# Optimization experiments

Measured on AMD Instinct MI355X. Metric: run time of the kernel, lower is better.

The kernel has to match this reference:

```python
import jax, jax.numpy as jnp
import numpy as np
import math

BS, N_AGENTS, TOPK = 256, 64, 8
IN_DIM, HID, ATT, N_ACT = 128, 256, 64, 16


def setup_inputs() -> dict:
    key = jax.random.key(0)
    ks = jax.random.split(key, 20)
    s = 0.05
    return {
        "inputs": jax.random.normal(ks[0], (BS * N_AGENTS, IN_DIM), jnp.float32),
        "hidden_state": jax.random.normal(ks[1], (BS * N_AGENTS, HID), jnp.float32),
        "msg": jax.random.normal(ks[2], (BS * N_AGENTS, HID), jnp.float32),
        "topk_indices": jax.random.randint(ks[3], (BS, N_AGENTS, TOPK), 0, N_AGENTS, jnp.int32),
        "fc1_w": jax.random.normal(ks[4], (HID, IN_DIM), jnp.float32) * s,
        "fc1_b": jnp.zeros((HID,), jnp.float32),
        "gru_w_ih": jax.random.normal(ks[5], (3 * HID, HID), jnp.float32) * s,
        "gru_b_ih": jnp.zeros((3 * HID,), jnp.float32),
        "gru_w_hh": jax.random.normal(ks[6], (3 * HID, HID), jnp.float32) * s,
        "gru_b_hh": jnp.zeros((3 * HID,), jnp.float32),
        "q_w": jax.random.normal(ks[7], (ATT, HID), jnp.float32) * s,
        "q_b": jnp.zeros((ATT,), jnp.float32),
        "k_w": jax.random.normal(ks[8], (ATT, HID), jnp.float32) * s,
        "k_b": jnp.zeros((ATT,), jnp.float32),
        "v_w": jax.random.normal(ks[9], (HID, HID), jnp.float32) * s,
        "v_b": jnp.zeros((HID,), jnp.float32),
        "fc2a_w": jax.random.normal(ks[10], (HID, 2 * HID), jnp.float32) * s,
        "fc2a_b": jnp.zeros((HID,), jnp.float32),
        "fc2b_w": jax.random.normal(ks[11], (N_ACT, HID), jnp.float32) * s,
        "fc2b_b": jnp.zeros((N_ACT,), jnp.float32),
    }


def _forward(inputs, hidden_state, msg, topk_indices,
             fc1_w, fc1_b, gru_w_ih, gru_b_ih, gru_w_hh, gru_b_hh,
             q_w, q_b, k_w, k_b, v_w, v_b, fc2a_w, fc2a_b, fc2b_w, fc2b_b):
    # fc1 + ReLU
    x = jax.nn.relu(inputs @ fc1_w.T + fc1_b)  # [B*N, HID]
    # GRUCell (torch semantics)
    gi = x @ gru_w_ih.T + gru_b_ih             # [B*N, 3H]
    gh = hidden_state @ gru_w_hh.T + gru_b_hh
    i_r, i_z, i_n = jnp.split(gi, 3, axis=-1)
    h_r, h_z, h_n = jnp.split(gh, 3, axis=-1)
    r = jax.nn.sigmoid(i_r + h_r)
    z = jax.nn.sigmoid(i_z + h_z)
    n = jnp.tanh(i_n + r * h_n)
    h = (1.0 - z) * n + z * hidden_state       # [B*N, HID]

    # communicate: gather top-k neighbor messages, attend, aggregate
    msg_r = msg.reshape(BS, N_AGENTS, HID)
    msg_received = jax.vmap(lambda m, idx: m[idx])(msg_r, topk_indices)  # [B,N,K,HID]
    ego_h = h.reshape(BS, N_AGENTS, HID)
    q = ego_h @ q_w.T + q_b                    # [B,N,ATT]
    k = msg_received @ k_w.T + k_b             # [B,N,K,ATT]
    logits = jnp.einsum('bnka,bna->bnk', k, q) / math.sqrt(ATT)
    attn = jax.nn.softmax(logits, axis=-1)     # [B,N,K]
    m = msg_received @ v_w.T + v_b             # [B,N,K,HID]
    m_agg = jnp.einsum('bnk,bnkh->bnh', attn, m).reshape(BS * N_AGENTS, HID)

    out = jnp.concatenate([h, m_agg], axis=-1)  # [B*N, 2H]
    q_out = jax.nn.relu(out @ fc2a_w.T + fc2a_b) @ fc2b_w.T + fc2b_b  # [B*N, N_ACT]
    return q_out, h, m_agg


def reference(inputs, hidden_state, msg, topk_indices,
              fc1_w, fc1_b, gru_w_ih, gru_b_ih, gru_w_hh, gru_b_hh,
              q_w, q_b, k_w, k_b, v_w, v_b, fc2a_w, fc2a_b, fc2b_w, fc2b_b):
    return _forward(inputs, hidden_state, msg, topk_indices,
                    fc1_w, fc1_b, gru_w_ih, gru_b_ih, gru_w_hh, gru_b_hh,
                    q_w, q_b, k_w, k_b, v_w, v_b, fc2a_w, fc2a_b, fc2b_w, fc2b_b)
```

## Files before the change

### kernel.cpp

```cpp
#include <hip/hip_runtime.h>

typedef __bf16 bf16;
typedef __attribute__((ext_vector_type(8))) __bf16 bf16x8;
typedef __attribute__((ext_vector_type(4))) __bf16 bf16x4;
typedef __attribute__((ext_vector_type(4))) float f32x4;

static constexpr int ROWS = 16384;

static constexpr size_t OFF_WFC1 = 0;
static constexpr size_t OFF_WRX  = 32768;
static constexpr size_t OFF_WZX  = 98304;
static constexpr size_t OFF_WNI  = 163840;
static constexpr size_t OFF_WRH  = 229376;
static constexpr size_t OFF_WZH  = 294912;
static constexpr size_t OFF_WNH  = 360448;
static constexpr size_t OFF_WQ   = 425984;
static constexpr size_t OFF_WKV  = 442368;
static constexpr size_t OFF_F2AH = 524288;
static constexpr size_t OFF_F2AM = 589824;
static constexpr size_t OFF_WF2B = 655360;

struct SwzSeg { const float* src; bf16* dst; int items; int k8s; int k32; int ld; };
struct SwzArgs { SwzSeg seg[14]; int count; };

__global__ __launch_bounds__(256) void swz_k(SwzArgs a) {
    const int tid = blockIdx.x * 256 + threadIdx.x;
    const int stride = gridDim.x * 256;
    for (int s = 0; s < a.count; ++s) {
        const float* __restrict__ src = a.seg[s].src;
        bf16* __restrict__ dst = a.seg[s].dst;
        const int items = a.seg[s].items, k8s = a.seg[s].k8s;
        const int k32c = a.seg[s].k32, ld = a.seg[s].ld;
        for (int i = tid; i < items; i += stride) {
            const int n = i >> k8s, kb = i & ((1 << k8s) - 1);
            const int k0 = kb << 3;
            const int lane = (n & 15) | ((kb & 3) << 4);
            const size_t off = ((size_t)((n >> 4) * k32c + (kb >> 2)) * 64 + lane) * 8;
            const float* p = src + (size_t)n * ld + k0;
            float4 f0 = *(const float4*)p;
            float4 f1 = *(const float4*)(p + 4);
            bf16x8 o = { (bf16)f0.x, (bf16)f0.y, (bf16)f0.z, (bf16)f0.w,
                         (bf16)f1.x, (bf16)f1.y, (bf16)f1.z, (bf16)f1.w };
            *(bf16x8*)(dst + off) = o;
        }
    }
}

template<int FM, int FN, int K32>
__device__ __forceinline__ void mm_swz(f32x4 (&acc)[FM][FN],
    const bf16* __restrict__ sA, int lda,
    const bf16* __restrict__ W, int lane)
{
    const int lr = lane & 15, lk = (lane >> 4) << 3;
    #pragma unroll
    for (int k32 = 0; k32 < K32; ++k32) {
        bf16x8 a[FM], b[FN];
        #pragma unroll
        for (int j = 0; j < FN; ++j)
            b[j] = *(const bf16x8*)(W + ((size_t)(j * K32 + k32) * 64 + lane) * 8);
        #pragma unroll
        for (int i = 0; i < FM; ++i)
            a[i] = *(const bf16x8*)&sA[(i * 16 + lr) * lda + k32 * 32 + lk];
        #pragma unroll
        for (int i = 0; i < FM; ++i)
            #pragma unroll
            for (int j = 0; j < FN; ++j)
                acc[i][j] = __builtin_amdgcn_mfma_f32_16x16x32_bf16(a[i], b[j], acc[i][j], 0, 0, 0);
    }
}

__device__ __forceinline__ void gate3(f32x4 (&g1)[4], f32x4 (&g2)[4], f32x4 (&g3)[4],
    const bf16* __restrict__ sA,
    const bf16* __restrict__ p1, const bf16* __restrict__ p2,
    const bf16* __restrict__ p3, int lane)
{
    const int lr = lane & 15, lk = (lane >> 4) << 3;
    const int lo = lane * 8;
    bf16x8 c1 = *(const bf16x8*)(p1 + lo);
    bf16x8 c2 = *(const bf16x8*)(p2 + lo);
    bf16x8 c3 = *(const bf16x8*)(p3 + lo);
    #pragma unroll
    for (int k = 0; k < 8; ++k) {
        bf16x8 n1, n2, n3;
        if (k < 7) {
            n1 = *(const bf16x8*)(p1 + (k + 1) * 512 + lo);
            n2 = *(const bf16x8*)(p2 + (k + 1) * 512 + lo);
            n3 = *(const bf16x8*)(p3 + (k + 1) * 512 + lo);
        }
        #pragma unroll
        for (int i = 0; i < 4; ++i) {
            bf16x8 a = *(const bf16x8*)&sA[(i * 16 + lr) * 264 + k * 32 + lk];
            g1[i] = __builtin_amdgcn_mfma_f32_16x16x32_bf16(a, c1, g1[i], 0, 0, 0);
            g2[i] = __builtin_amdgcn_mfma_f32_16x16x32_bf16(a, c2, g2[i], 0, 0, 0);
            g3[i] = __builtin_amdgcn_mfma_f32_16x16x32_bf16(a, c3, g3[i], 0, 0, 0);
        }
        if (k < 7) { c1 = n1; c2 = n2; c3 = n3; }
    }
}

__device__ __forceinline__ float sigmf(float x) { return 1.f / (1.f + __expf(-x)); }
__device__ __forceinline__ float tanh_fast(float x) {
    x = fminf(fmaxf(x, -15.f), 15.f);
    float e2 = __expf(2.f * x);
    return (e2 - 1.f) / (e2 + 1.f);
}

__global__ __launch_bounds__(1024)
void mega_k(const float* __restrict__ in_f, const float* __restrict__ hid_f,
            const float* __restrict__ msg_f, const int* __restrict__ topk,
            const bf16* __restrict__ Wfc1, const float* __restrict__ fc1_b,
            const bf16* __restrict__ WrX, const bf16* __restrict__ WrH,
            const bf16* __restrict__ WzX, const bf16* __restrict__ WzH,
            const bf16* __restrict__ Wni, const bf16* __restrict__ Wnh,
            const float* __restrict__ b_ih, const float* __restrict__ b_hh,
            const bf16* __restrict__ Wq, const float* __restrict__ q_b,
            const bf16* __restrict__ Wkv, const float* __restrict__ v_bias,
            const bf16* __restrict__ f2aH, const bf16* __restrict__ f2aM,
            const float* __restrict__ f2a_b,
            const bf16* __restrict__ Wf2b, const float* __restrict__ f2b_b,
            float* __restrict__ h_out, float* __restrict__ magg_out,
            float* __restrict__ q_out)
{
    __shared__ bf16 sH[64 * 264];
    __shared__ bf16 sB[64 * 264];
    __shared__ bf16 sG[64 * 264];
    __shared__ bf16 sM[64 * 264];
    __shared__ bf16 sQ[64 * 72];
    __shared__ bf16 sK[64 * 72];
    __shared__ int  sIdx[512];
    const int tid = threadIdx.x;
    const int wave = tid >> 6, lane = tid & 63;
    const int b64 = blockIdx.x * 64;
    const int lr = lane & 15, l4 = (lane >> 4) << 2, lk = (lane >> 4) << 3;

    #pragma unroll
    for (int c = tid; c < 4096; c += 1024) {
        int r = c >> 6, cg = (c & 63) << 2;
        float4 f = *(const float4*)(hid_f + (size_t)(b64 + r) * 256 + cg);
        float4 g = *(const float4*)(msg_f + (size_t)(b64 + r) * 256 + cg);
        bf16x4 oh = { (bf16)f.x, (bf16)f.y, (bf16)f.z, (bf16)f.w };
        bf16x4 og = { (bf16)g.x, (bf16)g.y, (bf16)g.z, (bf16)g.w };
        *(bf16x4*)&sH[r * 264 + cg] = oh;
        *(bf16x4*)&sG[r * 264 + cg] = og;
    }
    if (tid < 512) sIdx[tid] = topk[(size_t)blockIdx.x * 512 + tid];

    {
        f32x4 fa[4] = {};
        const float* ap = in_f + (size_t)(b64 + (wave & 3) * 16 + lr) * 128 + lk;
        const bf16*  wp = Wfc1 + (size_t)(wave >> 2) * 16 * 512 + lane * 8;
        #pragma unroll
        for (int k = 0; k < 4; ++k) {
            float4 f0 = *(const float4*)(ap + k * 32);
            float4 f1 = *(const float4*)(ap + k * 32 + 4);
            bf16x8 af = { (bf16)f0.x, (bf16)f0.y, (bf16)f0.z, (bf16)f0.w,
                          (bf16)f1.x, (bf16)f1.y, (bf16)f1.z, (bf16)f1.w };
            #pragma unroll
            for (int j = 0; j < 4; ++j) {
                bf16x8 bfr = *(const bf16x8*)(wp + (size_t)(j * 4 + k) * 512);
                fa[j] = __builtin_amdgcn_mfma_f32_16x16x32_bf16(af, bfr, fa[j], 0, 0, 0);
            }
        }
        #pragma unroll
        for (int j = 0; j < 4; ++j) {
            const int col = (wave >> 2) * 64 + j * 16 + lr;
            const float bv = fc1_b[col];
            #pragma unroll
            for (int rr = 0; rr < 4; ++rr)
                sB[((wave & 3) * 16 + l4 + rr) * 264 + col] = (bf16)fmaxf(fa[j][rr] + bv, 0.f);
        }
    }
    __syncthreads();

    const size_t nb = (size_t)wave * 8 * 512;
    f32x4 rg[4] = {}, zg[4] = {}, ng[4] = {}, hg[4] = {};
    gate3(rg, zg, hg, sH, WrH + nb, WzH + nb, Wnh + nb, lane);
    gate3(rg, zg, ng, sB, WrX + nb, WzX + nb, Wni + nb, lane);

    {
        const int col = wave * 16 + lr;
        const float br = b_ih[col] + b_hh[col];
        const float bz = b_ih[256 + col] + b_hh[256 + col];
        const float bi = b_ih[512 + col], bh = b_hh[512 + col];
        #pragma unroll
        for (int i = 0; i < 4; ++i)
            #pragma unroll
            for (int rr = 0; rr < 4; ++rr) {
                const int row = i * 16 + l4 + rr;
                const float rv = sigmf(rg[i][rr] + br);
                const float zv = sigmf(zg[i][rr] + bz);
                const float nn = tanh_fast((ng[i][rr] + bi) + rv * (hg[i][rr] + bh));
                const float hd = (float)sH[row * 264 + col];
                const float h = (1.f - zv) * nn + zv * hd;
                h_out[(size_t)(b64 + row) * 256 + col] = h;
                sM[row * 264 + col] = (bf16)h;
            }
    }
    __syncthreads();

    if (wave < 4) {
        f32x4 a[4][2] = {};
        mm_swz<4, 2, 8>(a, sG, 264, Wkv + (size_t)(wave * 2) * 8 * 512, lane);
        #pragma unroll
        for (int i = 0; i < 4; ++i)
            #pragma unroll
            for (int j = 0; j < 2; ++j) {
                const int col = (wave * 2 + j) * 16 + lr;
                #pragma unroll
                for (int rr = 0; rr < 4; ++rr) {
                    const int row = i * 16 + l4 + rr;
                    if (col < 64) sK[row * 72 + col] = (bf16)a[i][j][rr];
                    else          sB[row * 264 + col - 64] = (bf16)a[i][j][rr];
                }
            }
    } else {
        f32x4 a[4][1] = {};
        mm_swz<4, 1, 8>(a, sG, 264, Wkv + (size_t)(4 + wave) * 8 * 512, lane);
        const int col = (4 + wave) * 16 + lr;
        #pragma unroll
        for (int i = 0; i < 4; ++i)
            #pragma unroll
            for (int rr = 0; rr < 4; ++rr)
                sB[(i * 16 + l4 + rr) * 264 + col - 64] = (bf16)a[i][0][rr];
    }
    {
        f32x4 qa[1][1] = {};
        mm_swz<1, 1, 8>(qa, sM + (wave & 3) * 16 * 264, 264,
                        Wq + (size_t)(wave >> 2) * 8 * 512, lane);
        const int col = (wave >> 2) * 16 + lr;
        const float bv = q_b[col];
        #pragma unroll
        for (int rr = 0; rr < 4; ++rr)
            sQ[((wave & 3) * 16 + l4 + rr) * 72 + col] = (bf16)(qa[0][0][rr] + bv);
    }
    __syncthreads();

    const int kk = lane >> 3, dg = lane & 7;
    #pragma unroll
    for (int uu = 0; uu < 4; ++uu) {
        const int u = wave * 4 + uu;
        const int rowk = sIdx[u * 8 + kk];
        bf16x8 q8 = *(const bf16x8*)&sQ[u * 72 + dg * 8];
        bf16x8 k8 = *(const bf16x8*)&sK[rowk * 72 + dg * 8];
        float s = 0.f;
        #pragma unroll
        for (int t = 0; t < 8; ++t) s += (float)q8[t] * (float)k8[t];
        s += __shfl_xor(s, 1); s += __shfl_xor(s, 2); s += __shfl_xor(s, 4);
        float logit = s * 0.125f;
        float mx = logit;
        mx = fmaxf(mx, __shfl_xor(mx, 8));
        mx = fmaxf(mx, __shfl_xor(mx, 16));
        mx = fmaxf(mx, __shfl_xor(mx, 32));
        float e = __expf(logit - mx);
        float den = e;
        den += __shfl_xor(den, 8); den += __shfl_xor(den, 16); den += __shfl_xor(den, 32);
        const float wv = e / den;
        float a0 = 0.f, a1 = 0.f, a2 = 0.f, a3 = 0.f;
        #pragma unroll
        for (int k = 0; k < 8; ++k) {
            float wk = __shfl(wv, k * 8);
            int   rk = __shfl(rowk, k * 8);
            bf16x4 v = *(const bf16x4*)&sB[rk * 264 + lane * 4];
            a0 += wk * (float)v[0]; a1 += wk * (float)v[1];
            a2 += wk * (float)v[2]; a3 += wk * (float)v[3];
        }
        float4 vb = *(const float4*)(v_bias + lane * 4);
        a0 += vb.x; a1 += vb.y; a2 += vb.z; a3 += vb.w;
        float4 res = { a0, a1, a2, a3 };
        *(float4*)(magg_out + (size_t)(b64 + u) * 256 + lane * 4) = res;
        bf16x4 rb = { (bf16)a0, (bf16)a1, (bf16)a2, (bf16)a3 };
        *(bf16x4*)&sH[u * 264 + lane * 4] = rb;
    }
    __syncthreads();

    {
        f32x4 ya[4] = {};
        const bf16* pH = f2aH + nb;
        const bf16* pM = f2aM + nb;
        const int lo = lane * 8;
        bf16x8 cH = *(const bf16x8*)(pH + lo);
        bf16x8 cM = *(const bf16x8*)(pM + lo);
        #pragma unroll
        for (int k = 0; k < 8; ++k) {
            bf16x8 nH, nM;
            if (k < 7) {
                nH = *(const bf16x8*)(pH + (k + 1) * 512 + lo);
                nM = *(const bf16x8*)(pM + (k + 1) * 512 + lo);
            }
            #pragma unroll
            for (int i = 0; i < 4; ++i) {
                bf16x8 aH = *(const bf16x8*)&sM[(i * 16 + lr) * 264 + k * 32 + lk];
                bf16x8 aM = *(const bf16x8*)&sH[(i * 16 + lr) * 264 + k * 32 + lk];
                ya[i] = __builtin_amdgcn_mfma_f32_16x16x32_bf16(aH, cH, ya[i], 0, 0, 0);
                ya[i] = __builtin_amdgcn_mfma_f32_16x16x32_bf16(aM, cM, ya[i], 0, 0, 0);
            }
            if (k < 7) { cH = nH; cM = nM; }
        }
        const int col = wave * 16 + lr;
        const float bv = f2a_b[col];
        #pragma unroll
        for (int i = 0; i < 4; ++i)
            #pragma unroll
            for (int rr = 0; rr < 4; ++rr)
                sG[(i * 16 + l4 + rr) * 264 + col] = (bf16)fmaxf(ya[i][rr] + bv, 0.f);
    }
    __syncthreads();

    if (wave < 4) {
        f32x4 acc[1][1] = {};
        mm_swz<1, 1, 8>(acc, sG + wave * 16 * 264, 264, Wf2b, lane);
        const float bv = f2b_b[lr];
        #pragma unroll
        for (int rr = 0; rr < 4; ++rr)
            q_out[(size_t)(b64 + wave * 16 + l4 + rr) * 16 + lr] = acc[0][0][rr] + bv;
    }
}

extern "C" void kernel_launch(void* const* d_in, const int* in_sizes, int n_in,
                              void* d_out, int out_size, void* d_ws, size_t ws_size,
                              hipStream_t stream)
{
    const float* in_f   = (const float*)d_in[0];
    const float* hid_f  = (const float*)d_in[1];
    const float* msg_f  = (const float*)d_in[2];
    const int*   topk   = (const int*)d_in[3];
    const float* fc1w_f = (const float*)d_in[4];
    const float* fc1_b  = (const float*)d_in[5];
    const float* wih_f  = (const float*)d_in[6];
    const float* b_ih   = (const float*)d_in[7];
    const float* whh_f  = (const float*)d_in[8];
    const float* b_hh   = (const float*)d_in[9];
    const float* qw_f   = (const float*)d_in[10];
    const float* q_b    = (const float*)d_in[11];
    const float* kw_f   = (const float*)d_in[12];
    const float* vw_f   = (const float*)d_in[14];
    const float* v_b    = (const float*)d_in[15];
    const float* f2aw_f = (const float*)d_in[16];
    const float* f2a_b  = (const float*)d_in[17];
    const float* f2bw_f = (const float*)d_in[18];
    const float* f2b_b  = (const float*)d_in[19];

    bf16* ws = (bf16*)d_ws;
    bf16* Wfc1 = ws + OFF_WFC1;
    bf16* WrX  = ws + OFF_WRX;
    bf16* WzX  = ws + OFF_WZX;
    bf16* Wni  = ws + OFF_WNI;
    bf16* WrH  = ws + OFF_WRH;
    bf16* WzH  = ws + OFF_WZH;
    bf16* Wnh  = ws + OFF_WNH;
    bf16* Wq   = ws + OFF_WQ;
    bf16* Wkv  = ws + OFF_WKV;
    bf16* f2aH = ws + OFF_F2AH;
    bf16* f2aM = ws + OFF_F2AM;
    bf16* Wf2b = ws + OFF_WF2B;

    float* q_out    = (float*)d_out;
    float* h_out    = q_out + (size_t)ROWS * 16;
    float* magg_out = h_out + (size_t)ROWS * 256;

    SwzArgs sa{};
    int s = 0;
    auto add = [&](const float* src, bf16* dst, int N, int K, int ld) {
        sa.seg[s].src = src; sa.seg[s].dst = dst;
        sa.seg[s].items = N * (K >> 3);
        sa.seg[s].k8s = (K == 128) ? 4 : 5;
        sa.seg[s].k32 = K >> 5;
        sa.seg[s].ld = ld; ++s;
    };
    add(fc1w_f,          Wfc1, 256, 128, 128);
    add(wih_f,           WrX,  256, 256, 256);
    add(wih_f +  65536,  WzX,  256, 256, 256);
    add(wih_f + 131072,  Wni,  256, 256, 256);
    add(whh_f,           WrH,  256, 256, 256);
    add(whh_f +  65536,  WzH,  256, 256, 256);
    add(whh_f + 131072,  Wnh,  256, 256, 256);
    add(qw_f,            Wq,    64, 256, 256);
    add(kw_f,            Wkv,   64, 256, 256);
    add(vw_f,            Wkv + 16384, 256, 256, 256);
    add(f2aw_f,          f2aH, 256, 256, 512);
    add(f2aw_f + 256,    f2aM, 256, 256, 512);
    add(f2bw_f,          Wf2b,  16, 256, 256);
    sa.count = s;
    swz_k<<<256, 256, 0, stream>>>(sa);

    mega_k<<<256, 1024, 0, stream>>>(in_f, hid_f, msg_f, topk,
                                     Wfc1, fc1_b, WrX, WrH, WzX, WzH, Wni, Wnh,
                                     b_ih, b_hh, Wq, q_b, Wkv, v_b,
                                     f2aH, f2aM, f2a_b, Wf2b, f2b_b,
                                     h_out, magg_out, q_out);
}
```

Before: 56.69 us.

## Split GRU gate GEMMs into r/z and n phases, deepen weight prefetch

Restructures the GRU gate computation into two phases. The first accumulates only r and z and packs their sigmoids into bf16 pairs. The second computes the n-gate input and hidden products using a two-stage-deep weight prefetch. The input activation loads for fc1 are issued at kernel start to overlap with the hidden/msg staging, and the fc2a loop gains the same double-depth prefetch. The aim is to lower peak accumulator register pressure (fewer live f32x4 arrays) and hide global weight-load latency. The cost is that r and z are stored in bf16, which loses some precision.

```diff
diff --git a/kernel.cpp b/kernel.cpp
--- a/kernel.cpp
+++ b/kernel.cpp
@@ -69,40 +69,22 @@
     }
 }
 
-__device__ __forceinline__ void gate3(f32x4 (&g1)[4], f32x4 (&g2)[4], f32x4 (&g3)[4],
-    const bf16* __restrict__ sA,
-    const bf16* __restrict__ p1, const bf16* __restrict__ p2,
-    const bf16* __restrict__ p3, int lane)
-{
-    const int lr = lane & 15, lk = (lane >> 4) << 3;
-    const int lo = lane * 8;
-    bf16x8 c1 = *(const bf16x8*)(p1 + lo);
-    bf16x8 c2 = *(const bf16x8*)(p2 + lo);
-    bf16x8 c3 = *(const bf16x8*)(p3 + lo);
-    #pragma unroll
-    for (int k = 0; k < 8; ++k) {
-        bf16x8 n1, n2, n3;
-        if (k < 7) {
-            n1 = *(const bf16x8*)(p1 + (k + 1) * 512 + lo);
-            n2 = *(const bf16x8*)(p2 + (k + 1) * 512 + lo);
-            n3 = *(const bf16x8*)(p3 + (k + 1) * 512 + lo);
-        }
-        #pragma unroll
-        for (int i = 0; i < 4; ++i) {
-            bf16x8 a = *(const bf16x8*)&sA[(i * 16 + lr) * 264 + k * 32 + lk];
-            g1[i] = __builtin_amdgcn_mfma_f32_16x16x32_bf16(a, c1, g1[i], 0, 0, 0);
-            g2[i] = __builtin_amdgcn_mfma_f32_16x16x32_bf16(a, c2, g2[i], 0, 0, 0);
-            g3[i] = __builtin_amdgcn_mfma_f32_16x16x32_bf16(a, c3, g3[i], 0, 0, 0);
-        }
-        if (k < 7) { c1 = n1; c2 = n2; c3 = n3; }
-    }
-}
-
 __device__ __forceinline__ float sigmf(float x) { return 1.f / (1.f + __expf(-x)); }
 __device__ __forceinline__ float tanh_fast(float x) {
     x = fminf(fmaxf(x, -15.f), 15.f);
     float e2 = __expf(2.f * x);
     return (e2 - 1.f) / (e2 + 1.f);
+}
+__device__ __forceinline__ unsigned pk_bf16(float a, float b) {
+    unsigned short ua = __builtin_bit_cast(unsigned short, (bf16)a);
+    unsigned short ub = __builtin_bit_cast(unsigned short, (bf16)b);
+    return (unsigned)ua | ((unsigned)ub << 16);
+}
+__device__ __forceinline__ float unpk_lo(unsigned p) {
+    return (float)__builtin_bit_cast(bf16, (unsigned short)(p & 0xffff));
+}
+__device__ __forceinline__ float unpk_hi(unsigned p) {
+    return (float)__builtin_bit_cast(bf16, (unsigned short)(p >> 16));
 }
 
 __global__ __launch_bounds__(1024)
@@ -133,6 +115,16 @@
     const int b64 = blockIdx.x * 64;
     const int lr = lane & 15, l4 = (lane >> 4) << 2, lk = (lane >> 4) << 3;
 
+    float4 inA[8];
+    {
+        const float* ap = in_f + (size_t)(b64 + (wave & 3) * 16 + lr) * 128 + lk;
+        #pragma unroll
+        for (int k = 0; k < 4; ++k) {
+            inA[2 * k]     = *(const float4*)(ap + k * 32);
+            inA[2 * k + 1] = *(const float4*)(ap + k * 32 + 4);
+        }
+    }
+
     #pragma unroll
     for (int c = tid; c < 4096; c += 1024) {
         int r = c >> 6, cg = (c & 63) << 2;
@@ -147,12 +139,10 @@
 
     {
         f32x4 fa[4] = {};
-        const float* ap = in_f + (size_t)(b64 + (wave & 3) * 16 + lr) * 128 + lk;
-        const bf16*  wp = Wfc1 + (size_t)(wave >> 2) * 16 * 512 + lane * 8;
+        const bf16* wp = Wfc1 + (size_t)(wave >> 2) * 16 * 512 + lane * 8;
         #pragma unroll
         for (int k = 0; k < 4; ++k) {
-            float4 f0 = *(const float4*)(ap + k * 32);
-            float4 f1 = *(const float4*)(ap + k * 32 + 4);
+            float4 f0 = inA[2 * k], f1 = inA[2 * k + 1];
             bf16x8 af = { (bf16)f0.x, (bf16)f0.y, (bf16)f0.z, (bf16)f0.w,
                           (bf16)f1.x, (bf16)f1.y, (bf16)f1.z, (bf16)f1.w };
             #pragma unroll
@@ -173,22 +163,81 @@
     __syncthreads();
 
     const size_t nb = (size_t)wave * 8 * 512;
-    f32x4 rg[4] = {}, zg[4] = {}, ng[4] = {}, hg[4] = {};
-    gate3(rg, zg, hg, sH, WrH + nb, WzH + nb, Wnh + nb, lane);
-    gate3(rg, zg, ng, sB, WrX + nb, WzX + nb, Wni + nb, lane);
-
-    {
+    const int lo = lane * 8;
+    unsigned rz_pk[16];
+    {
+        const bf16 *pRX = WrX + nb + lo, *pZX = WzX + nb + lo;
+        const bf16 *pRH = WrH + nb + lo, *pZH = WzH + nb + lo;
+        f32x4 rg[4] = {}, zg[4] = {};
+        bf16x8 cRX = *(const bf16x8*)pRX, cZX = *(const bf16x8*)pZX;
+        bf16x8 cRH = *(const bf16x8*)pRH, cZH = *(const bf16x8*)pZH;
+        #pragma unroll
+        for (int k = 0; k < 8; ++k) {
+            bf16x8 nRX, nZX, nRH, nZH;
+            if (k < 7) {
+                nRX = *(const bf16x8*)(pRX + (k + 1) * 512);
+                nZX = *(const bf16x8*)(pZX + (k + 1) * 512);
+                nRH = *(const bf16x8*)(pRH + (k + 1) * 512);
+                nZH = *(const bf16x8*)(pZH + (k + 1) * 512);
+            }
+            #pragma unroll
+            for (int i = 0; i < 4; ++i) {
+                bf16x8 ax = *(const bf16x8*)&sB[(i * 16 + lr) * 264 + k * 32 + lk];
+                rg[i] = __builtin_amdgcn_mfma_f32_16x16x32_bf16(ax, cRX, rg[i], 0, 0, 0);
+                zg[i] = __builtin_amdgcn_mfma_f32_16x16x32_bf16(ax, cZX, zg[i], 0, 0, 0);
+            }
+            #pragma unroll
+            for (int i = 0; i < 4; ++i) {
+                bf16x8 ah = *(const bf16x8*)&sH[(i * 16 + lr) * 264 + k * 32 + lk];
+                rg[i] = __builtin_amdgcn_mfma_f32_16x16x32_bf16(ah, cRH, rg[i], 0, 0, 0);
+                zg[i] = __builtin_amdgcn_mfma_f32_16x16x32_bf16(ah, cZH, zg[i], 0, 0, 0);
+            }
+            if (k < 7) { cRX = nRX; cZX = nZX; cRH = nRH; cZH = nZH; }
+        }
         const int col = wave * 16 + lr;
         const float br = b_ih[col] + b_hh[col];
         const float bz = b_ih[256 + col] + b_hh[256 + col];
+        #pragma unroll
+        for (int i = 0; i < 4; ++i)
+            #pragma unroll
+            for (int rr = 0; rr < 4; ++rr)
+                rz_pk[i * 4 + rr] = pk_bf16(sigmf(rg[i][rr] + br), sigmf(zg[i][rr] + bz));
+    }
+
+    {
+        const bf16 *pNI = Wni + nb + lo, *pNH = Wnh + nb + lo;
+        f32x4 ng[4] = {}, hg[4] = {};
+        bf16x8 c0 = *(const bf16x8*)pNI,         c1 = *(const bf16x8*)pNH;
+        bf16x8 d0 = *(const bf16x8*)(pNI + 512), d1 = *(const bf16x8*)(pNH + 512);
+        #pragma unroll
+        for (int k = 0; k < 8; ++k) {
+            bf16x8 e0, e1;
+            if (k < 6) {
+                e0 = *(const bf16x8*)(pNI + (k + 2) * 512);
+                e1 = *(const bf16x8*)(pNH + (k + 2) * 512);
+            }
+            #pragma unroll
+            for (int i = 0; i < 4; ++i) {
+                bf16x8 ax = *(const bf16x8*)&sB[(i * 16 + lr) * 264 + k * 32 + lk];
+                ng[i] = __builtin_amdgcn_mfma_f32_16x16x32_bf16(ax, c0, ng[i], 0, 0, 0);
+            }
+            #pragma unroll
+            for (int i = 0; i < 4; ++i) {
+                bf16x8 ah = *(const bf16x8*)&sH[(i * 16 + lr) * 264 + k * 32 + lk];
+                hg[i] = __builtin_amdgcn_mfma_f32_16x16x32_bf16(ah, c1, hg[i], 0, 0, 0);
+            }
+            c0 = d0; c1 = d1;
+            if (k < 6) { d0 = e0; d1 = e1; }
+        }
+        const int col = wave * 16 + lr;
         const float bi = b_ih[512 + col], bh = b_hh[512 + col];
         #pragma unroll
         for (int i = 0; i < 4; ++i)
             #pragma unroll
             for (int rr = 0; rr < 4; ++rr) {
                 const int row = i * 16 + l4 + rr;
-                const float rv = sigmf(rg[i][rr] + br);
-                const float zv = sigmf(zg[i][rr] + bz);
+                const unsigned p = rz_pk[i * 4 + rr];
+                const float rv = unpk_lo(p), zv = unpk_hi(p);
                 const float nn = tanh_fast((ng[i][rr] + bi) + rv * (hg[i][rr] + bh));
                 const float hd = (float)sH[row * 264 + col];
                 const float h = (1.f - zv) * nn + zv * hd;
@@ -275,26 +324,29 @@
 
     {
         f32x4 ya[4] = {};
-        const bf16* pH = f2aH + nb;
-        const bf16* pM = f2aM + nb;
-        const int lo = lane * 8;
-        bf16x8 cH = *(const bf16x8*)(pH + lo);
-        bf16x8 cM = *(const bf16x8*)(pM + lo);
+        const bf16* pH = f2aH + nb + lo;
+        const bf16* pM = f2aM + nb + lo;
+        bf16x8 cH = *(const bf16x8*)pH,         cM = *(const bf16x8*)pM;
+        bf16x8 dH = *(const bf16x8*)(pH + 512), dM = *(const bf16x8*)(pM + 512);
         #pragma unroll
         for (int k = 0; k < 8; ++k) {
-            bf16x8 nH, nM;
-            if (k < 7) {
-                nH = *(const bf16x8*)(pH + (k + 1) * 512 + lo);
-                nM = *(const bf16x8*)(pM + (k + 1) * 512 + lo);
+            bf16x8 eH, eM;
+            if (k < 6) {
+                eH = *(const bf16x8*)(pH + (k + 2) * 512);
+                eM = *(const bf16x8*)(pM + (k + 2) * 512);
             }
             #pragma unroll
             for (int i = 0; i < 4; ++i) {
                 bf16x8 aH = *(const bf16x8*)&sM[(i * 16 + lr) * 264 + k * 32 + lk];
+                ya[i] = __builtin_amdgcn_mfma_f32_16x16x32_bf16(aH, cH, ya[i], 0, 0, 0);
+            }
+            #pragma unroll
+            for (int i = 0; i < 4; ++i) {
                 bf16x8 aM = *(const bf16x8*)&sH[(i * 16 + lr) * 264 + k * 32 + lk];
-                ya[i] = __builtin_amdgcn_mfma_f32_16x16x32_bf16(aH, cH, ya[i], 0, 0, 0);
                 ya[i] = __builtin_amdgcn_mfma_f32_16x16x32_bf16(aM, cM, ya[i], 0, 0, 0);
             }
-            if (k < 7) { cH = nH; cM = nM; }
+            cH = dH; cM = dM;
+            if (k < 6) { dH = eH; dM = eM; }
         }
         const int col = wave * 16 + lr;
         const float bv = f2a_b[col];
```

New measurement: 59.19 us. +4.4%, slower.

## Retile GRU and fc2a GEMMs to 32x32 per wave and reorder global loads

Applied to the files above, without the earlier changes.

Each wave now computes a 2x2 grid of 16x16 MFMA tiles (32 rows by 32 cols) for the GRU gates and fc2a, instead of 64 rows by 16 cols. This reuses each A and B fragment twice and cuts redundant LDS and weight reads. The input and msg global loads are issued earlier to hide their latency: msg is converted to LDS between the two gate passes, and s_setprio is raised around the MFMA bursts. h_out is now written with coalesced float4 stores read back from the bf16 copy in LDS, so the h output loses precision to bf16 rounding.

```diff
diff --git a/kernel.cpp b/kernel.cpp
--- a/kernel.cpp
+++ b/kernel.cpp
@@ -69,32 +69,36 @@
     }
 }
 
-__device__ __forceinline__ void gate3(f32x4 (&g1)[4], f32x4 (&g2)[4], f32x4 (&g3)[4],
-    const bf16* __restrict__ sA,
+__device__ __forceinline__ void gate3_32(f32x4 (&g1)[2][2], f32x4 (&g2)[2][2], f32x4 (&g3)[2][2],
+    const bf16* __restrict__ sA, int rowbase,
     const bf16* __restrict__ p1, const bf16* __restrict__ p2,
     const bf16* __restrict__ p3, int lane)
 {
     const int lr = lane & 15, lk = (lane >> 4) << 3;
-    const int lo = lane * 8;
-    bf16x8 c1 = *(const bf16x8*)(p1 + lo);
-    bf16x8 c2 = *(const bf16x8*)(p2 + lo);
-    bf16x8 c3 = *(const bf16x8*)(p3 + lo);
     #pragma unroll
     for (int k = 0; k < 8; ++k) {
-        bf16x8 n1, n2, n3;
-        if (k < 7) {
-            n1 = *(const bf16x8*)(p1 + (k + 1) * 512 + lo);
-            n2 = *(const bf16x8*)(p2 + (k + 1) * 512 + lo);
-            n3 = *(const bf16x8*)(p3 + (k + 1) * 512 + lo);
-        }
-        #pragma unroll
-        for (int i = 0; i < 4; ++i) {
-            bf16x8 a = *(const bf16x8*)&sA[(i * 16 + lr) * 264 + k * 32 + lk];
-            g1[i] = __builtin_amdgcn_mfma_f32_16x16x32_bf16(a, c1, g1[i], 0, 0, 0);
-            g2[i] = __builtin_amdgcn_mfma_f32_16x16x32_bf16(a, c2, g2[i], 0, 0, 0);
-            g3[i] = __builtin_amdgcn_mfma_f32_16x16x32_bf16(a, c3, g3[i], 0, 0, 0);
-        }
-        if (k < 7) { c1 = n1; c2 = n2; c3 = n3; }
+        bf16x8 a0 = *(const bf16x8*)&sA[(rowbase + lr) * 264 + k * 32 + lk];
+        bf16x8 a1 = *(const bf16x8*)&sA[(rowbase + 16 + lr) * 264 + k * 32 + lk];
+        bf16x8 b10 = *(const bf16x8*)(p1 + k * 512);
+        bf16x8 b11 = *(const bf16x8*)(p1 + 4096 + k * 512);
+        bf16x8 b20 = *(const bf16x8*)(p2 + k * 512);
+        bf16x8 b21 = *(const bf16x8*)(p2 + 4096 + k * 512);
+        bf16x8 b30 = *(const bf16x8*)(p3 + k * 512);
+        bf16x8 b31 = *(const bf16x8*)(p3 + 4096 + k * 512);
+        __builtin_amdgcn_s_setprio(1);
+        g1[0][0] = __builtin_amdgcn_mfma_f32_16x16x32_bf16(a0, b10, g1[0][0], 0, 0, 0);
+        g1[0][1] = __builtin_amdgcn_mfma_f32_16x16x32_bf16(a0, b11, g1[0][1], 0, 0, 0);
+        g1[1][0] = __builtin_amdgcn_mfma_f32_16x16x32_bf16(a1, b10, g1[1][0], 0, 0, 0);
+        g1[1][1] = __builtin_amdgcn_mfma_f32_16x16x32_bf16(a1, b11, g1[1][1], 0, 0, 0);
+        g2[0][0] = __builtin_amdgcn_mfma_f32_16x16x32_bf16(a0, b20, g2[0][0], 0, 0, 0);
+        g2[0][1] = __builtin_amdgcn_mfma_f32_16x16x32_bf16(a0, b21, g2[0][1], 0, 0, 0);
+        g2[1][0] = __builtin_amdgcn_mfma_f32_16x16x32_bf16(a1, b20, g2[1][0], 0, 0, 0);
+        g2[1][1] = __builtin_amdgcn_mfma_f32_16x16x32_bf16(a1, b21, g2[1][1], 0, 0, 0);
+        g3[0][0] = __builtin_amdgcn_mfma_f32_16x16x32_bf16(a0, b30, g3[0][0], 0, 0, 0);
+        g3[0][1] = __builtin_amdgcn_mfma_f32_16x16x32_bf16(a0, b31, g3[0][1], 0, 0, 0);
+        g3[1][0] = __builtin_amdgcn_mfma_f32_16x16x32_bf16(a1, b30, g3[1][0], 0, 0, 0);
+        g3[1][1] = __builtin_amdgcn_mfma_f32_16x16x32_bf16(a1, b31, g3[1][1], 0, 0, 0);
+        __builtin_amdgcn_s_setprio(0);
     }
 }
 
@@ -132,27 +136,33 @@
     const int wave = tid >> 6, lane = tid & 63;
     const int b64 = blockIdx.x * 64;
     const int lr = lane & 15, l4 = (lane >> 4) << 2, lk = (lane >> 4) << 3;
-
+    const int wm = wave >> 3, wn = wave & 7;
+
+    float4 inA[8];
+    {
+        const float* ap = in_f + (size_t)(b64 + (wave & 3) * 16 + lr) * 128 + lk;
+        #pragma unroll
+        for (int k = 0; k < 4; ++k) {
+            inA[2 * k]     = *(const float4*)(ap + k * 32);
+            inA[2 * k + 1] = *(const float4*)(ap + k * 32 + 4);
+        }
+    }
     #pragma unroll
     for (int c = tid; c < 4096; c += 1024) {
         int r = c >> 6, cg = (c & 63) << 2;
         float4 f = *(const float4*)(hid_f + (size_t)(b64 + r) * 256 + cg);
-        float4 g = *(const float4*)(msg_f + (size_t)(b64 + r) * 256 + cg);
         bf16x4 oh = { (bf16)f.x, (bf16)f.y, (bf16)f.z, (bf16)f.w };
-        bf16x4 og = { (bf16)g.x, (bf16)g.y, (bf16)g.z, (bf16)g.w };
         *(bf16x4*)&sH[r * 264 + cg] = oh;
-        *(bf16x4*)&sG[r * 264 + cg] = og;
     }
     if (tid < 512) sIdx[tid] = topk[(size_t)blockIdx.x * 512 + tid];
+    __syncthreads();
 
     {
         f32x4 fa[4] = {};
-        const float* ap = in_f + (size_t)(b64 + (wave & 3) * 16 + lr) * 128 + lk;
-        const bf16*  wp = Wfc1 + (size_t)(wave >> 2) * 16 * 512 + lane * 8;
+        const bf16* wp = Wfc1 + (size_t)(wave >> 2) * 16 * 512 + lane * 8;
         #pragma unroll
         for (int k = 0; k < 4; ++k) {
-            float4 f0 = *(const float4*)(ap + k * 32);
-            float4 f1 = *(const float4*)(ap + k * 32 + 4);
+            float4 f0 = inA[2 * k], f1 = inA[2 * k + 1];
             bf16x8 af = { (bf16)f0.x, (bf16)f0.y, (bf16)f0.z, (bf16)f0.w,
                           (bf16)f1.x, (bf16)f1.y, (bf16)f1.z, (bf16)f1.w };
             #pragma unroll
@@ -170,32 +180,47 @@
                 sB[((wave & 3) * 16 + l4 + rr) * 264 + col] = (bf16)fmaxf(fa[j][rr] + bv, 0.f);
         }
     }
-    __syncthreads();
-
-    const size_t nb = (size_t)wave * 8 * 512;
-    f32x4 rg[4] = {}, zg[4] = {}, ng[4] = {}, hg[4] = {};
-    gate3(rg, zg, hg, sH, WrH + nb, WzH + nb, Wnh + nb, lane);
-    gate3(rg, zg, ng, sB, WrX + nb, WzX + nb, Wni + nb, lane);
-
-    {
-        const int col = wave * 16 + lr;
-        const float br = b_ih[col] + b_hh[col];
-        const float bz = b_ih[256 + col] + b_hh[256 + col];
-        const float bi = b_ih[512 + col], bh = b_hh[512 + col];
-        #pragma unroll
-        for (int i = 0; i < 4; ++i)
+
+    float4 mr[4];
+    #pragma unroll
+    for (int u = 0; u < 4; ++u) {
+        int c = tid + u * 1024;
+        mr[u] = *(const float4*)(msg_f + (size_t)(b64 + (c >> 6)) * 256 + ((c & 63) << 2));
+    }
+
+    const size_t nb = (size_t)(wn * 2) * 8 * 512 + lane * 8;
+    f32x4 rg[2][2] = {}, zg[2][2] = {}, ng[2][2] = {}, hg[2][2] = {};
+    gate3_32(rg, zg, hg, sH, wm * 32, WrH + nb, WzH + nb, Wnh + nb, lane);
+
+    #pragma unroll
+    for (int u = 0; u < 4; ++u) {
+        int c = tid + u * 1024;
+        bf16x4 og = { (bf16)mr[u].x, (bf16)mr[u].y, (bf16)mr[u].z, (bf16)mr[u].w };
+        *(bf16x4*)&sG[(c >> 6) * 264 + ((c & 63) << 2)] = og;
+    }
+    __syncthreads();
+
+    gate3_32(rg, zg, ng, sB, wm * 32, WrX + nb, WzX + nb, Wni + nb, lane);
+
+    #pragma unroll
+    for (int i = 0; i < 2; ++i)
+        #pragma unroll
+        for (int j = 0; j < 2; ++j) {
+            const int col = wn * 32 + j * 16 + lr;
+            const float br = b_ih[col] + b_hh[col];
+            const float bz = b_ih[256 + col] + b_hh[256 + col];
+            const float bi = b_ih[512 + col], bh = b_hh[512 + col];
             #pragma unroll
             for (int rr = 0; rr < 4; ++rr) {
-                const int row = i * 16 + l4 + rr;
-                const float rv = sigmf(rg[i][rr] + br);
-                const float zv = sigmf(zg[i][rr] + bz);
-                const float nn = tanh_fast((ng[i][rr] + bi) + rv * (hg[i][rr] + bh));
+                const int row = wm * 32 + i * 16 + l4 + rr;
+                const float rv = sigmf(rg[i][j][rr] + br);
+                const float zv = sigmf(zg[i][j][rr] + bz);
+                const float nn = tanh_fast((ng[i][j][rr] + bi) + rv * (hg[i][j][rr] + bh));
                 const float hd = (float)sH[row * 264 + col];
                 const float h = (1.f - zv) * nn + zv * hd;
-                h_out[(size_t)(b64 + row) * 256 + col] = h;
                 sM[row * 264 + col] = (bf16)h;
             }
-    }
+        }
     __syncthreads();
 
     if (wave < 4) {
@@ -233,6 +258,14 @@
         for (int rr = 0; rr < 4; ++rr)
             sQ[((wave & 3) * 16 + l4 + rr) * 72 + col] = (bf16)(qa[0][0][rr] + bv);
     }
+    #pragma unroll
+    for (int u = 0; u < 4; ++u) {
+        int c = tid + u * 1024;
+        int r = c >> 6, cg = (c & 63) << 2;
+        bf16x4 hv = *(const bf16x4*)&sM[r * 264 + cg];
+        float4 o = { (float)hv[0], (float)hv[1], (float)hv[2], (float)hv[3] };
+        *(float4*)(h_out + (size_t)(b64 + r) * 256 + cg) = o;
+    }
     __syncthreads();
 
     const int kk = lane >> 3, dg = lane & 7;
@@ -274,35 +307,40 @@
     __syncthreads();
 
     {
-        f32x4 ya[4] = {};
+        f32x4 ya[2][2] = {};
         const bf16* pH = f2aH + nb;
         const bf16* pM = f2aM + nb;
-        const int lo = lane * 8;
-        bf16x8 cH = *(const bf16x8*)(pH + lo);
-        bf16x8 cM = *(const bf16x8*)(pM + lo);
         #pragma unroll
         for (int k = 0; k < 8; ++k) {
-            bf16x8 nH, nM;
-            if (k < 7) {
-                nH = *(const bf16x8*)(pH + (k + 1) * 512 + lo);
-                nM = *(const bf16x8*)(pM + (k + 1) * 512 + lo);
+            bf16x8 aH0 = *(const bf16x8*)&sM[(wm * 32 + lr) * 264 + k * 32 + lk];
+            bf16x8 aH1 = *(const bf16x8*)&sM[(wm * 32 + 16 + lr) * 264 + k * 32 + lk];
+            bf16x8 aM0 = *(const bf16x8*)&sH[(wm * 32 + lr) * 264 + k * 32 + lk];
+            bf16x8 aM1 = *(const bf16x8*)&sH[(wm * 32 + 16 + lr) * 264 + k * 32 + lk];
+            bf16x8 bH0 = *(const bf16x8*)(pH + k * 512);
+            bf16x8 bH1 = *(const bf16x8*)(pH + 4096 + k * 512);
+            bf16x8 bM0 = *(const bf16x8*)(pM + k * 512);
+            bf16x8 bM1 = *(const bf16x8*)(pM + 4096 + k * 512);
+            __builtin_amdgcn_s_setprio(1);
+            ya[0][0] = __builtin_amdgcn_mfma_f32_16x16x32_bf16(aH0, bH0, ya[0][0], 0, 0, 0);
+            ya[0][1] = __builtin_amdgcn_mfma_f32_16x16x32_bf16(aH0, bH1, ya[0][1], 0, 0, 0);
+            ya[1][0] = __builtin_amdgcn_mfma_f32_16x16x32_bf16(aH1, bH0, ya[1][0], 0, 0, 0);
+            ya[1][1] = __builtin_amdgcn_mfma_f32_16x16x32_bf16(aH1, bH1, ya[1][1], 0, 0, 0);
+            ya[0][0] = __builtin_amdgcn_mfma_f32_16x16x32_bf16(aM0, bM0, ya[0][0], 0, 0, 0);
+            ya[0][1] = __builtin_amdgcn_mfma_f32_16x16x32_bf16(aM0, bM1, ya[0][1], 0, 0, 0);
+            ya[1][0] = __builtin_amdgcn_mfma_f32_16x16x32_bf16(aM1, bM0, ya[1][0], 0, 0, 0);
+            ya[1][1] = __builtin_amdgcn_mfma_f32_16x16x32_bf16(aM1, bM1, ya[1][1], 0, 0, 0);
+            __builtin_amdgcn_s_setprio(0);
+        }
+        #pragma unroll
+        for (int i = 0; i < 2; ++i)
+            #pragma unroll
+            for (int j = 0; j < 2; ++j) {
+                const int col = wn * 32 + j * 16 + lr;
+                const float bv = f2a_b[col];
+                #pragma unroll
+                for (int rr = 0; rr < 4; ++rr)
+                    sG[(wm * 32 + i * 16 + l4 + rr) * 264 + col] = (bf16)fmaxf(ya[i][j][rr] + bv, 0.f);
             }
-            #pragma unroll
-            for (int i = 0; i < 4; ++i) {
-                bf16x8 aH = *(const bf16x8*)&sM[(i * 16 + lr) * 264 + k * 32 + lk];
-                bf16x8 aM = *(const bf16x8*)&sH[(i * 16 + lr) * 264 + k * 32 + lk];
-                ya[i] = __builtin_amdgcn_mfma_f32_16x16x32_bf16(aH, cH, ya[i], 0, 0, 0);
-                ya[i] = __builtin_amdgcn_mfma_f32_16x16x32_bf16(aM, cM, ya[i], 0, 0, 0);
-            }
-            if (k < 7) { cH = nH; cM = nM; }
-        }
-        const int col = wave * 16 + lr;
-        const float bv = f2a_b[col];
-        #pragma unroll
-        for (int i = 0; i < 4; ++i)
-            #pragma unroll
-            for (int rr = 0; rr < 4; ++rr)
-                sG[(i * 16 + l4 + rr) * 264 + col] = (bf16)fmaxf(ya[i][rr] + bv, 0.f);
     }
     __syncthreads();
 
```

Result: slower. 62.96 us (+11.1%).
